# Kernel tuning notes

Hardware: AMD Instinct MI355X
Metric: run time of the kernel (lower is better)

## Reference

```python
import jax, jax.numpy as jnp
import numpy as np

ITERATION = 3
NEG = -2.0**16 + 1.0  # mask fill value from the torch code


def setup_inputs() -> dict:
    key = jax.random.key(0)
    k1, k2, k3, k4 = jax.random.split(key, 4)
    B, L, D_in, D_out, K = 1024, 512, 64, 64, 8
    low_capsule = jax.random.normal(k1, (B, L, D_in), dtype=jnp.float32)
    B_init = jax.random.normal(k2, (1, K, L), dtype=jnp.float32)
    S = jax.random.normal(k3, (D_in, D_out), dtype=jnp.float32)
    seq_len = jax.random.randint(k4, (B, 1), 1, L + 1, dtype=jnp.int32)
    return {"low_capsule": low_capsule, "B_init": B_init, "S": S, "seq_len": seq_len}


def _squash(x):
    # torch code sums squared norm over dim=1 (the capsule/max_k dim), keepdim
    sq = jnp.sum(jnp.square(x), axis=1, keepdims=True)
    scale = sq / (1.0 + sq) / jnp.sqrt(sq + 1e-9)
    return scale * x


def reference(low_capsule, B_init, S, seq_len):
    # low_capsule: [B, L, D_in], B_init: [1, K, L], S: [D_in, D_out], seq_len: [B, 1]
    Bsz, L, _ = low_capsule.shape
    K = B_init.shape[1]
    # sequence mask: [B, K, L] (seq_len tiled over K)
    mask = jnp.arange(L, dtype=seq_len.dtype)[None, None, :] < seq_len[:, :, None]
    mask = jnp.broadcast_to(mask, (Bsz, K, L))
    # bilinear projection is loop-invariant; compute once
    low_new = jnp.einsum('bld,do->blo', low_capsule, S)  # [B, L, D_out]
    B_mat = B_init
    high = None
    for _ in range(ITERATION):
        logits = jnp.where(mask, B_mat, NEG)               # [B, K, L]
        W = jax.nn.softmax(logits, axis=-1)                # masked softmax
        high = _squash(jnp.einsum('bkl,blo->bko', W, low_new))  # [B, K, D_out]
        B_delta = jnp.sum(jnp.einsum('bko,blo->bkl', high, low_new),
                          axis=0, keepdims=True)           # [1, K, L]
        B_mat = B_mat + B_delta
    return high
```

## Files before the change

### kernel.cpp

```cpp
#include <hip/hip_runtime.h>

#define NEG_FILL (-65535.0f)
#define NSLOT 32

typedef __attribute__((ext_vector_type(8))) short  short8;
typedef __attribute__((ext_vector_type(4))) float  floatx4;

__device__ inline unsigned short f2bf(float f) {
    unsigned u = __float_as_uint(f);
    u += 0x7FFFu + ((u >> 16) & 1u);
    return (unsigned short)(u >> 16);
}
__device__ inline float bf2f(unsigned short h) {
    return __uint_as_float(((unsigned)h) << 16);
}

__global__ __launch_bounds__(256) void k_init(const float* __restrict__ Binit,
                                              float* __restrict__ B0,
                                              float* __restrict__ slots) {
    int i = blockIdx.x * 256 + threadIdx.x;
    slots[i] = 0.f;
    if (i < 4096) B0[i] = Binit[i];
}

__global__ __launch_bounds__(256) void k_bred(const float* __restrict__ Bcur,
                                              float* __restrict__ Bnext,
                                              float* __restrict__ slots) {
    int i = blockIdx.x * 256 + threadIdx.x;
    float s = Bcur[i];
    #pragma unroll
    for (int j = 0; j < NSLOT; ++j) {
        s += slots[j * 4096 + i];
        slots[j * 4096 + i] = 0.f;
    }
    Bnext[i] = s;
}

__device__ __forceinline__ void softmax_to_WsT(
    const float* __restrict__ Bc, int sl, int lane, int g,
    float (*WsT)[8]) {
    #pragma unroll
    for (int kk = 0; kk < 2; ++kk) {
        const int k = g + (kk << 2);
        float v[8];
        float mx = NEG_FILL;
        #pragma unroll
        for (int j = 0; j < 8; ++j) {
            int l = lane + (j << 6);
            v[j] = (l < sl) ? Bc[(k << 9) + l] : NEG_FILL;
            mx = fmaxf(mx, v[j]);
        }
        #pragma unroll
        for (int off = 32; off; off >>= 1) mx = fmaxf(mx, __shfl_xor(mx, off));
        float s = 0.f;
        #pragma unroll
        for (int j = 0; j < 8; ++j) { v[j] = expf(v[j] - mx); s += v[j]; }
        #pragma unroll
        for (int off = 32; off; off >>= 1) s += __shfl_xor(s, off);
        const float inv = 1.0f / s;
        #pragma unroll
        for (int j = 0; j < 8; ++j) WsT[lane + (j << 6)][k] = v[j] * inv;
    }
}

__device__ __forceinline__ void delta_phase(
    const unsigned short* __restrict__ lnb, const unsigned short (*Hn)[64],
    float* __restrict__ slot, int g, int m, int q) {
    short8 afragH[2];
    #pragma unroll
    for (int oh = 0; oh < 2; ++oh) {
        short8 f = {0, 0, 0, 0, 0, 0, 0, 0};
        if (m < 8) f = *(const short8*)&Hn[m][oh * 32 + q * 8];
        afragH[oh] = f;
    }
    #pragma unroll
    for (int half = 0; half < 2; ++half) {
        short8 bf[4][2];
        #pragma unroll
        for (int t2 = 0; t2 < 4; ++t2) {
            const int lt = (g << 7) + (((half << 2) + t2) << 4);
            const unsigned short* p = &lnb[((lt + m) << 6) + q * 8];
            bf[t2][0] = *(const short8*)p;
            bf[t2][1] = *(const short8*)(p + 32);
        }
        #pragma unroll
        for (int t2 = 0; t2 < 4; ++t2) {
            const int lt = (g << 7) + (((half << 2) + t2) << 4);
            floatx4 acc = {0.f, 0.f, 0.f, 0.f};
            acc = __builtin_amdgcn_mfma_f32_16x16x32_bf16(afragH[0], bf[t2][0], acc, 0, 0, 0);
            acc = __builtin_amdgcn_mfma_f32_16x16x32_bf16(afragH[1], bf[t2][1], acc, 0, 0, 0);
            if (q < 2) {
                #pragma unroll
                for (int r = 0; r < 4; ++r)
                    atomicAdd(&slot[(q * 4 + r) * 512 + lt + m], acc[r]);
            }
        }
    }
}

__global__ __launch_bounds__(256, 4) void k_fused0(
    const float* __restrict__ low,
    const float* __restrict__ S,
    const float* __restrict__ Bc,
    float* __restrict__ slots,
    const int* __restrict__ seq_len,
    unsigned short* __restrict__ ln)
{
    __shared__ __align__(16) float WsT[512][8];
    __shared__ __align__(16) float Tpart[4][8][64];
    __shared__ __align__(16) float Tred[8][64];
    __shared__ __align__(16) unsigned short Hn[8][64];

    const int t = threadIdx.x, lane = t & 63, g = t >> 6, b = blockIdx.x;
    const int m = lane & 15, q = lane >> 4;
    const int sl = seq_len[b];
    const float* lowb = low + ((size_t)b << 15);
    unsigned short* lnb = ln + ((size_t)b << 15);

    softmax_to_WsT(Bc, sl, lane, g, WsT);
    __syncthreads();

    short8 sfrag[4][2];
    #pragma unroll
    for (int nt = 0; nt < 4; ++nt)
        #pragma unroll
        for (int dh = 0; dh < 2; ++dh) {
            short8 f;
            #pragma unroll
            for (int j = 0; j < 8; ++j) {
                int d = dh * 32 + q * 8 + j;
                f[j] = (short)f2bf(S[(d << 6) + nt * 16 + m]);
            }
            sfrag[nt][dh] = f;
        }

    float Tp[8][4];
    #pragma unroll
    for (int k = 0; k < 8; ++k)
        #pragma unroll
        for (int nt = 0; nt < 4; ++nt) Tp[k][nt] = 0.f;

    for (int tt = 0; tt < 8; ++tt) {
        const int lt = (g << 7) + (tt << 4);
        short8 afrag[2];
        #pragma unroll
        for (int dh = 0; dh < 2; ++dh) {
            const float4* p =
                (const float4*)&lowb[((lt + m) << 6) + dh * 32 + q * 8];
            float4 x0 = p[0], x1 = p[1];
            short8 f;
            f[0] = (short)f2bf(x0.x); f[1] = (short)f2bf(x0.y);
            f[2] = (short)f2bf(x0.z); f[3] = (short)f2bf(x0.w);
            f[4] = (short)f2bf(x1.x); f[5] = (short)f2bf(x1.y);
            f[6] = (short)f2bf(x1.z); f[7] = (short)f2bf(x1.w);
            afrag[dh] = f;
        }
        float lnr[4][4];
        #pragma unroll
        for (int nt = 0; nt < 4; ++nt) {
            floatx4 acc = {0.f, 0.f, 0.f, 0.f};
            acc = __builtin_amdgcn_mfma_f32_16x16x32_bf16(afrag[0], sfrag[nt][0], acc, 0, 0, 0);
            acc = __builtin_amdgcn_mfma_f32_16x16x32_bf16(afrag[1], sfrag[nt][1], acc, 0, 0, 0);
            #pragma unroll
            for (int r = 0; r < 4; ++r) {
                unsigned short hb = f2bf(acc[r]);
                lnb[((size_t)(lt + (q << 2) + r) << 6) + nt * 16 + m] = hb;
                lnr[r][nt] = bf2f(hb);
            }
        }
        if (lt < sl) {
            #pragma unroll
            for (int r = 0; r < 4; ++r) {
                const int l = lt + (q << 2) + r;
                const float4 wa = *(const float4*)&WsT[l][0];
                const float4 wb = *(const float4*)&WsT[l][4];
                #pragma unroll
                for (int nt = 0; nt < 4; ++nt) {
                    const float x = lnr[r][nt];
                    Tp[0][nt] = fmaf(wa.x, x, Tp[0][nt]);
                    Tp[1][nt] = fmaf(wa.y, x, Tp[1][nt]);
                    Tp[2][nt] = fmaf(wa.z, x, Tp[2][nt]);
                    Tp[3][nt] = fmaf(wa.w, x, Tp[3][nt]);
                    Tp[4][nt] = fmaf(wb.x, x, Tp[4][nt]);
                    Tp[5][nt] = fmaf(wb.y, x, Tp[5][nt]);
                    Tp[6][nt] = fmaf(wb.z, x, Tp[6][nt]);
                    Tp[7][nt] = fmaf(wb.w, x, Tp[7][nt]);
                }
            }
        }
    }
    #pragma unroll
    for (int k = 0; k < 8; ++k)
        #pragma unroll
        for (int nt = 0; nt < 4; ++nt) {
            float v = Tp[k][nt];
            v += __shfl_xor(v, 16);
            v += __shfl_xor(v, 32);
            Tp[k][nt] = v;
        }
    #pragma unroll
    for (int k = 0; k < 8; ++k) Tpart[g][k][lane] = Tp[k][q];
    __syncthreads();

    #pragma unroll
    for (int idx = t; idx < 512; idx += 256) {
        float s = (&Tpart[0][0][0])[idx] + (&Tpart[1][0][0])[idx]
                + (&Tpart[2][0][0])[idx] + (&Tpart[3][0][0])[idx];
        (&Tred[0][0])[idx] = s;
    }
    __syncthreads();

    float sq = 0.f;
    #pragma unroll
    for (int k = 0; k < 8; ++k) { float x = Tred[k][lane]; sq = fmaf(x, x, sq); }
    const float scale = sq / (1.0f + sq) / sqrtf(sq + 1e-9f);
    Hn[g][lane]     = f2bf(scale * Tred[g][lane]);
    Hn[g + 4][lane] = f2bf(scale * Tred[g + 4][lane]);
    __syncthreads();

    delta_phase(lnb, Hn, slots + ((size_t)(b & (NSLOT - 1)) << 12), g, m, q);
}

__global__ __launch_bounds__(256, 4) void k_route2(
    const unsigned short* __restrict__ ln,
    const float* __restrict__ Bc,
    float* __restrict__ slots,
    const int* __restrict__ seq_len,
    float* __restrict__ out,
    int last)
{
    __shared__ __align__(16) float WsT[512][8];
    __shared__ __align__(16) float Tpart[4][8][64];
    __shared__ __align__(16) float Tred[8][64];
    __shared__ __align__(16) unsigned short Hn[8][64];

    const int t = threadIdx.x, lane = t & 63, g = t >> 6, b = blockIdx.x;
    const int m = lane & 15, q = lane >> 4;
    const int sl = seq_len[b];
    const unsigned short* lnb = ln + ((size_t)b << 15);

    softmax_to_WsT(Bc, sl, lane, g, WsT);
    __syncthreads();

    floatx4 Tacc[8];
    #pragma unroll
    for (int k = 0; k < 8; ++k) Tacc[k] = (floatx4){0.f, 0.f, 0.f, 0.f};
    const int l0 = g << 7;
    const int rem = sl - l0;
    int nact = (rem <= 0) ? 0 : ((rem + 31) >> 5);
    if (nact > 4) nact = 4;

    for (int ii = 0; ii < nact; ++ii) {
        uint2 u[8];
        #pragma unroll
        for (int j = 0; j < 8; ++j) {
            const int l = l0 + (ii << 5) + (j << 2) + q;
            u[j] = *(const uint2*)&lnb[(l << 6) + (m << 2)];
        }
        #pragma unroll
        for (int j = 0; j < 8; ++j) {
            const int l = l0 + (ii << 5) + (j << 2) + q;
            const float x0 = __uint_as_float(u[j].x << 16);
            const float x1 = __uint_as_float(u[j].x & 0xFFFF0000u);
            const float x2 = __uint_as_float(u[j].y << 16);
            const float x3 = __uint_as_float(u[j].y & 0xFFFF0000u);
            const float4 wa = *(const float4*)&WsT[l][0];
            const float4 wb = *(const float4*)&WsT[l][4];
#define TROW(K, WV)                                          \
            Tacc[K][0] = fmaf(WV, x0, Tacc[K][0]);           \
            Tacc[K][1] = fmaf(WV, x1, Tacc[K][1]);           \
            Tacc[K][2] = fmaf(WV, x2, Tacc[K][2]);           \
            Tacc[K][3] = fmaf(WV, x3, Tacc[K][3]);
            TROW(0, wa.x) TROW(1, wa.y) TROW(2, wa.z) TROW(3, wa.w)
            TROW(4, wb.x) TROW(5, wb.y) TROW(6, wb.z) TROW(7, wb.w)
#undef TROW
        }
    }
    #pragma unroll
    for (int k = 0; k < 8; ++k)
        #pragma unroll
        for (int j = 0; j < 4; ++j) {
            float v = Tacc[k][j];
            v += __shfl_xor(v, 16);
            v += __shfl_xor(v, 32);
            Tacc[k][j] = v;
        }
    if (q == 0) {
        #pragma unroll
        for (int k = 0; k < 8; ++k)
            *(float4*)&Tpart[g][k][m << 2] =
                make_float4(Tacc[k][0], Tacc[k][1], Tacc[k][2], Tacc[k][3]);
    }
    __syncthreads();

    #pragma unroll
    for (int idx = t; idx < 512; idx += 256) {
        float s = (&Tpart[0][0][0])[idx] + (&Tpart[1][0][0])[idx]
                + (&Tpart[2][0][0])[idx] + (&Tpart[3][0][0])[idx];
        (&Tred[0][0])[idx] = s;
    }
    __syncthreads();

    float sq = 0.f;
    #pragma unroll
    for (int k = 0; k < 8; ++k) { float x = Tred[k][lane]; sq = fmaf(x, x, sq); }
    const float scale = sq / (1.0f + sq) / sqrtf(sq + 1e-9f);
    const float hf0 = scale * Tred[g][lane];
    const float hf1 = scale * Tred[g + 4][lane];

    if (last) {
        out[(((size_t)b * 8 + g)     << 6) + lane] = hf0;
        out[(((size_t)b * 8 + g + 4) << 6) + lane] = hf1;
        return;
    }
    Hn[g][lane]     = f2bf(hf0);
    Hn[g + 4][lane] = f2bf(hf1);
    __syncthreads();

    delta_phase(lnb, Hn, slots + ((size_t)(b & (NSLOT - 1)) << 12), g, m, q);
}

__global__ __launch_bounds__(256) void k_copy4k(const float* __restrict__ src,
                                                float* __restrict__ dst) {
    int i = blockIdx.x * 256 + threadIdx.x;
    dst[i] = src[i];
}

__global__ __launch_bounds__(256, 4) void k_route(
    const float* __restrict__ low, const float* __restrict__ S,
    const float* __restrict__ Bcur, float* __restrict__ Bnext,
    const int* __restrict__ seq_len, float* __restrict__ out, int last)
{
    __shared__ float smemA[64 * 65];
    __shared__ float Spad[64][65];
    __shared__ float GT[64][8];
    __shared__ float Tred[8][64];
    float* WsT = smemA;
    float (*Tpart)[8][64] = (float (*)[8][64])smemA;
    float (*tile)[65]     = (float (*)[65])smemA;

    const int t = threadIdx.x, o = t & 63, g = t >> 6, b = blockIdx.x;
    const int sl = seq_len[b];
    const float* lowb = low + ((size_t)b << 15);

    #pragma unroll
    for (int i = 0; i < 16; ++i) {
        int idx = t + (i << 8);
        Spad[idx >> 6][idx & 63] = S[idx];
    }
    #pragma unroll
    for (int kk = 0; kk < 2; ++kk) {
        const int k = g + (kk << 2);
        float v[8];
        float mx = NEG_FILL;
        #pragma unroll
        for (int j = 0; j < 8; ++j) {
            int l = o + (j << 6);
            v[j] = (l < sl) ? Bcur[(k << 9) + l] : NEG_FILL;
            mx = fmaxf(mx, v[j]);
        }
        #pragma unroll
        for (int off = 32; off; off >>= 1) mx = fmaxf(mx, __shfl_xor(mx, off));
        float s = 0.f;
        #pragma unroll
        for (int j = 0; j < 8; ++j) { v[j] = expf(v[j] - mx); s += v[j]; }
        #pragma unroll
        for (int off = 32; off; off >>= 1) s += __shfl_xor(s, off);
        const float inv = 1.0f / s;
        #pragma unroll
        for (int j = 0; j < 8; ++j) WsT[((o + (j << 6)) << 3) + k] = v[j] * inv;
    }
    __syncthreads();

    float Ta[8];
    #pragma unroll
    for (int k = 0; k < 8; ++k) Ta[k] = 0.f;
    {
        const int l0 = g << 7;
        #pragma unroll 4
        for (int i = 0; i < 128; ++i) {
            const int l = l0 + i;
            const float x = lowb[(l << 6) + o];
            const float4 wa = *(const float4*)&WsT[(l << 3)];
            const float4 wb = *(const float4*)&WsT[(l << 3) + 4];
            Ta[0] = fmaf(wa.x, x, Ta[0]); Ta[1] = fmaf(wa.y, x, Ta[1]);
            Ta[2] = fmaf(wa.z, x, Ta[2]); Ta[3] = fmaf(wa.w, x, Ta[3]);
            Ta[4] = fmaf(wb.x, x, Ta[4]); Ta[5] = fmaf(wb.y, x, Ta[5]);
            Ta[6] = fmaf(wb.z, x, Ta[6]); Ta[7] = fmaf(wb.w, x, Ta[7]);
        }
    }
    __syncthreads();
    #pragma unroll
    for (int k = 0; k < 8; ++k) Tpart[g][k][o] = Ta[k];
    __syncthreads();

    float h0 = 0.f, h1 = 0.f;
    #pragma unroll
    for (int gg = 0; gg < 4; ++gg) { h0 += Tpart[gg][g][o]; h1 += Tpart[gg][g + 4][o]; }
    Tred[g][o] = h0; Tred[g + 4][o] = h1;
    __syncthreads();

    float hp0 = 0.f, hp1 = 0.f;
    #pragma unroll
    for (int d = 0; d < 64; ++d) {
        const float sv = Spad[d][o];
        hp0 = fmaf(Tred[g][d], sv, hp0);
        hp1 = fmaf(Tred[g + 4][d], sv, hp1);
    }
    __syncthreads();
    Tred[g][o] = hp0; Tred[g + 4][o] = hp1;
    __syncthreads();

    float sq = 0.f;
    #pragma unroll
    for (int k = 0; k < 8; ++k) { float x = Tred[k][o]; sq = fmaf(x, x, sq); }
    const float scale = sq / (1.0f + sq) / sqrtf(sq + 1e-9f);
    const float hf0 = scale * hp0;
    const float hf1 = scale * hp1;

    if (last) {
        out[(((size_t)b * 8 + g)     << 6) + o] = hf0;
        out[(((size_t)b * 8 + g + 4) << 6) + o] = hf1;
        return;
    }
    __syncthreads();
    Tred[g][o] = hf0; Tred[g + 4][o] = hf1;
    __syncthreads();

    float g0 = 0.f, g1 = 0.f;
    #pragma unroll
    for (int oo = 0; oo < 64; ++oo) {
        const float sv = Spad[o][oo];
        g0 = fmaf(Tred[g][oo], sv, g0);
        g1 = fmaf(Tred[g + 4][oo], sv, g1);
    }
    GT[o][g] = g0; GT[o][g + 4] = g1;
    __syncthreads();

    for (int c = 0; c < 8; ++c) {
        const int lc = c << 6;
        #pragma unroll
        for (int r = 0; r < 16; ++r) {
            const int lr = (g << 4) + r;
            tile[lr][o] = lowb[((lc + lr) << 6) + o];
        }
        __syncthreads();
        float a0 = 0.f, a1 = 0.f;
        #pragma unroll
        for (int d = 0; d < 64; ++d) {
            const float x = tile[o][d];
            a0 = fmaf(GT[d][g], x, a0);
            a1 = fmaf(GT[d][g + 4], x, a1);
        }
        atomicAdd(&Bnext[(g << 9) + lc + o], a0);
        atomicAdd(&Bnext[((g + 4) << 9) + lc + o], a1);
        __syncthreads();
    }
}

extern "C" void kernel_launch(void* const* d_in, const int* in_sizes, int n_in,
                              void* d_out, int out_size, void* d_ws, size_t ws_size,
                              hipStream_t stream) {
    const float* low   = (const float*)d_in[0];
    const float* Binit = (const float*)d_in[1];
    const float* S     = (const float*)d_in[2];
    const int*   seq   = (const int*)d_in[3];
    float* outp = (float*)d_out;

    const size_t LN_BYTES   = (size_t)1024 * 512 * 64 * 2;
    const size_t SLOT_BYTES = (size_t)NSLOT * 4096 * sizeof(float);
    const size_t NEED = LN_BYTES + SLOT_BYTES + 2 * 4096 * sizeof(float);

    if (ws_size >= NEED) {
        unsigned short* lnw = (unsigned short*)d_ws;
        float* slots = (float*)((char*)d_ws + LN_BYTES);
        float* B0 = slots + (size_t)NSLOT * 4096;
        float* B1 = B0 + 4096;

        k_init<<<(NSLOT * 4096) / 256, 256, 0, stream>>>(Binit, B0, slots);

        k_fused0<<<1024, 256, 0, stream>>>(low, S, B0, slots, seq, lnw);
        k_bred<<<16, 256, 0, stream>>>(B0, B1, slots);

        k_route2<<<1024, 256, 0, stream>>>(lnw, B1, slots, seq, outp, 0);
        k_bred<<<16, 256, 0, stream>>>(B1, B0, slots);

        k_route2<<<1024, 256, 0, stream>>>(lnw, B0, nullptr, seq, outp, 1);
    } else {
        float* B0 = (float*)d_ws;
        float* B1 = B0 + 4096;
        k_copy4k<<<16, 256, 0, stream>>>(Binit, B0);
        k_copy4k<<<16, 256, 0, stream>>>(B0, B1);
        k_route<<<1024, 256, 0, stream>>>(low, S, B0, B1, seq, outp, 0);
        k_copy4k<<<16, 256, 0, stream>>>(B1, B0);
        k_route<<<1024, 256, 0, stream>>>(low, S, B1, B0, seq, outp, 0);
        k_route<<<1024, 256, 0, stream>>>(low, S, B0, nullptr, seq, outp, 1);
    }
}
```

Baseline: 295.7 us.

## Split delta phase into separate higher-occupancy kernel over half-sequence blocks

The B_delta computation moves out of the fused route kernels into a standalone k_delta kernel. It launches 2048 blocks, each covering half of a batch row's sequence, with launch bounds allowing 8 blocks per CU. The high capsules are written in fp32 to the output buffer and re-read and packed to bf16 by k_delta. The lt<sl guard in the projection kernel is also removed, so masked rows are accumulated unconditionally. This relies on softmax weights there being zero. The intent is better occupancy and parallelism for the atomic-heavy delta phase, at the cost of extra launches and an extra global round trip for the high capsules.

```diff
diff --git a/kernel.cpp b/kernel.cpp
--- a/kernel.cpp
+++ b/kernel.cpp
@@ -13,6 +13,14 @@
 }
 __device__ inline float bf2f(unsigned short h) {
     return __uint_as_float(((unsigned)h) << 16);
+}
+__device__ __forceinline__ short8 pack8(float4 a, float4 b) {
+    short8 f;
+    f[0] = (short)f2bf(a.x); f[1] = (short)f2bf(a.y);
+    f[2] = (short)f2bf(a.z); f[3] = (short)f2bf(a.w);
+    f[4] = (short)f2bf(b.x); f[5] = (short)f2bf(b.y);
+    f[6] = (short)f2bf(b.z); f[7] = (short)f2bf(b.w);
+    return f;
 }
 
 __global__ __launch_bounds__(256) void k_init(const float* __restrict__ Binit,
@@ -63,53 +71,17 @@
     }
 }
 
-__device__ __forceinline__ void delta_phase(
-    const unsigned short* __restrict__ lnb, const unsigned short (*Hn)[64],
-    float* __restrict__ slot, int g, int m, int q) {
-    short8 afragH[2];
-    #pragma unroll
-    for (int oh = 0; oh < 2; ++oh) {
-        short8 f = {0, 0, 0, 0, 0, 0, 0, 0};
-        if (m < 8) f = *(const short8*)&Hn[m][oh * 32 + q * 8];
-        afragH[oh] = f;
-    }
-    #pragma unroll
-    for (int half = 0; half < 2; ++half) {
-        short8 bf[4][2];
-        #pragma unroll
-        for (int t2 = 0; t2 < 4; ++t2) {
-            const int lt = (g << 7) + (((half << 2) + t2) << 4);
-            const unsigned short* p = &lnb[((lt + m) << 6) + q * 8];
-            bf[t2][0] = *(const short8*)p;
-            bf[t2][1] = *(const short8*)(p + 32);
-        }
-        #pragma unroll
-        for (int t2 = 0; t2 < 4; ++t2) {
-            const int lt = (g << 7) + (((half << 2) + t2) << 4);
-            floatx4 acc = {0.f, 0.f, 0.f, 0.f};
-            acc = __builtin_amdgcn_mfma_f32_16x16x32_bf16(afragH[0], bf[t2][0], acc, 0, 0, 0);
-            acc = __builtin_amdgcn_mfma_f32_16x16x32_bf16(afragH[1], bf[t2][1], acc, 0, 0, 0);
-            if (q < 2) {
-                #pragma unroll
-                for (int r = 0; r < 4; ++r)
-                    atomicAdd(&slot[(q * 4 + r) * 512 + lt + m], acc[r]);
-            }
-        }
-    }
-}
-
-__global__ __launch_bounds__(256, 4) void k_fused0(
+__global__ __launch_bounds__(256, 4) void k_lnT(
     const float* __restrict__ low,
     const float* __restrict__ S,
     const float* __restrict__ Bc,
-    float* __restrict__ slots,
     const int* __restrict__ seq_len,
-    unsigned short* __restrict__ ln)
+    unsigned short* __restrict__ ln,
+    float* __restrict__ hout)
 {
     __shared__ __align__(16) float WsT[512][8];
     __shared__ __align__(16) float Tpart[4][8][64];
     __shared__ __align__(16) float Tred[8][64];
-    __shared__ __align__(16) unsigned short Hn[8][64];
 
     const int t = threadIdx.x, lane = t & 63, g = t >> 6, b = blockIdx.x;
     const int m = lane & 15, q = lane >> 4;
@@ -168,24 +140,22 @@
                 lnr[r][nt] = bf2f(hb);
             }
         }
-        if (lt < sl) {
+        #pragma unroll
+        for (int r = 0; r < 4; ++r) {
+            const int l = lt + (q << 2) + r;
+            const float4 wa = *(const float4*)&WsT[l][0];
+            const float4 wb = *(const float4*)&WsT[l][4];
             #pragma unroll
-            for (int r = 0; r < 4; ++r) {
-                const int l = lt + (q << 2) + r;
-                const float4 wa = *(const float4*)&WsT[l][0];
-                const float4 wb = *(const float4*)&WsT[l][4];
-                #pragma unroll
-                for (int nt = 0; nt < 4; ++nt) {
-                    const float x = lnr[r][nt];
-                    Tp[0][nt] = fmaf(wa.x, x, Tp[0][nt]);
-                    Tp[1][nt] = fmaf(wa.y, x, Tp[1][nt]);
-                    Tp[2][nt] = fmaf(wa.z, x, Tp[2][nt]);
-                    Tp[3][nt] = fmaf(wa.w, x, Tp[3][nt]);
-                    Tp[4][nt] = fmaf(wb.x, x, Tp[4][nt]);
-                    Tp[5][nt] = fmaf(wb.y, x, Tp[5][nt]);
-                    Tp[6][nt] = fmaf(wb.z, x, Tp[6][nt]);
-                    Tp[7][nt] = fmaf(wb.w, x, Tp[7][nt]);
-                }
+            for (int nt = 0; nt < 4; ++nt) {
+                const float x = lnr[r][nt];
+                Tp[0][nt] = fmaf(wa.x, x, Tp[0][nt]);
+                Tp[1][nt] = fmaf(wa.y, x, Tp[1][nt]);
+                Tp[2][nt] = fmaf(wa.z, x, Tp[2][nt]);
+                Tp[3][nt] = fmaf(wa.w, x, Tp[3][nt]);
+                Tp[4][nt] = fmaf(wb.x, x, Tp[4][nt]);
+                Tp[5][nt] = fmaf(wb.y, x, Tp[5][nt]);
+                Tp[6][nt] = fmaf(wb.z, x, Tp[6][nt]);
+                Tp[7][nt] = fmaf(wb.w, x, Tp[7][nt]);
             }
         }
     }
@@ -214,25 +184,19 @@
     #pragma unroll
     for (int k = 0; k < 8; ++k) { float x = Tred[k][lane]; sq = fmaf(x, x, sq); }
     const float scale = sq / (1.0f + sq) / sqrtf(sq + 1e-9f);
-    Hn[g][lane]     = f2bf(scale * Tred[g][lane]);
-    Hn[g + 4][lane] = f2bf(scale * Tred[g + 4][lane]);
-    __syncthreads();
-
-    delta_phase(lnb, Hn, slots + ((size_t)(b & (NSLOT - 1)) << 12), g, m, q);
-}
-
-__global__ __launch_bounds__(256, 4) void k_route2(
+    hout[((size_t)b << 9) + (g << 6) + lane]       = scale * Tred[g][lane];
+    hout[((size_t)b << 9) + ((g + 4) << 6) + lane] = scale * Tred[g + 4][lane];
+}
+
+__global__ __launch_bounds__(256, 4) void k_T(
     const unsigned short* __restrict__ ln,
     const float* __restrict__ Bc,
-    float* __restrict__ slots,
     const int* __restrict__ seq_len,
-    float* __restrict__ out,
-    int last)
+    float* __restrict__ hout)
 {
     __shared__ __align__(16) float WsT[512][8];
     __shared__ __align__(16) float Tpart[4][8][64];
     __shared__ __align__(16) float Tred[8][64];
-    __shared__ __align__(16) unsigned short Hn[8][64];
 
     const int t = threadIdx.x, lane = t & 63, g = t >> 6, b = blockIdx.x;
     const int m = lane & 15, q = lane >> 4;
@@ -305,19 +269,56 @@
     #pragma unroll
     for (int k = 0; k < 8; ++k) { float x = Tred[k][lane]; sq = fmaf(x, x, sq); }
     const float scale = sq / (1.0f + sq) / sqrtf(sq + 1e-9f);
-    const float hf0 = scale * Tred[g][lane];
-    const float hf1 = scale * Tred[g + 4][lane];
-
-    if (last) {
-        out[(((size_t)b * 8 + g)     << 6) + lane] = hf0;
-        out[(((size_t)b * 8 + g + 4) << 6) + lane] = hf1;
-        return;
-    }
-    Hn[g][lane]     = f2bf(hf0);
-    Hn[g + 4][lane] = f2bf(hf1);
-    __syncthreads();
-
-    delta_phase(lnb, Hn, slots + ((size_t)(b & (NSLOT - 1)) << 12), g, m, q);
+    hout[((size_t)b << 9) + (g << 6) + lane]       = scale * Tred[g][lane];
+    hout[((size_t)b << 9) + ((g + 4) << 6) + lane] = scale * Tred[g + 4][lane];
+}
+
+__global__ __launch_bounds__(256, 8) void k_delta(
+    const unsigned short* __restrict__ ln,
+    const float* __restrict__ hout,
+    float* __restrict__ slots)
+{
+    const int t = threadIdx.x, lane = t & 63, g = t >> 6;
+    const int bb = blockIdx.x, b = bb >> 1, half = bb & 1;
+    const int m = lane & 15, q = lane >> 4;
+    const unsigned short* lnb = ln + ((size_t)b << 15);
+    const float* hb = hout + ((size_t)b << 9);
+    float* slot = slots + ((size_t)(b & (NSLOT - 1)) << 12);
+
+    short8 afragH[2];
+    #pragma unroll
+    for (int oh = 0; oh < 2; ++oh) {
+        short8 f = {0, 0, 0, 0, 0, 0, 0, 0};
+        if (m < 8) {
+            const float4* p = (const float4*)&hb[(m << 6) + oh * 32 + q * 8];
+            f = pack8(p[0], p[1]);
+        }
+        afragH[oh] = f;
+    }
+    const int lbase = (half << 8) + (g << 6);
+    #pragma unroll
+    for (int pp = 0; pp < 2; ++pp) {
+        short8 bf[2][2];
+        #pragma unroll
+        for (int u = 0; u < 2; ++u) {
+            const int lt = lbase + (((pp << 1) + u) << 4);
+            const unsigned short* p = &lnb[((lt + m) << 6) + q * 8];
+            bf[u][0] = *(const short8*)p;
+            bf[u][1] = *(const short8*)(p + 32);
+        }
+        #pragma unroll
+        for (int u = 0; u < 2; ++u) {
+            const int lt = lbase + (((pp << 1) + u) << 4);
+            floatx4 acc = {0.f, 0.f, 0.f, 0.f};
+            acc = __builtin_amdgcn_mfma_f32_16x16x32_bf16(afragH[0], bf[u][0], acc, 0, 0, 0);
+            acc = __builtin_amdgcn_mfma_f32_16x16x32_bf16(afragH[1], bf[u][1], acc, 0, 0, 0);
+            if (q < 2) {
+                #pragma unroll
+                for (int r = 0; r < 4; ++r)
+                    atomicAdd(&slot[((q << 2) + r) * 512 + lt + m], acc[r]);
+            }
+        }
+    }
 }
 
 __global__ __launch_bounds__(256) void k_copy4k(const float* __restrict__ src,
@@ -479,13 +480,15 @@
 
         k_init<<<(NSLOT * 4096) / 256, 256, 0, stream>>>(Binit, B0, slots);
 
-        k_fused0<<<1024, 256, 0, stream>>>(low, S, B0, slots, seq, lnw);
+        k_lnT<<<1024, 256, 0, stream>>>(low, S, B0, seq, lnw, outp);
+        k_delta<<<2048, 256, 0, stream>>>(lnw, outp, slots);
         k_bred<<<16, 256, 0, stream>>>(B0, B1, slots);
 
-        k_route2<<<1024, 256, 0, stream>>>(lnw, B1, slots, seq, outp, 0);
+        k_T<<<1024, 256, 0, stream>>>(lnw, B1, seq, outp);
+        k_delta<<<2048, 256, 0, stream>>>(lnw, outp, slots);
         k_bred<<<16, 256, 0, stream>>>(B1, B0, slots);
 
-        k_route2<<<1024, 256, 0, stream>>>(lnw, B0, nullptr, seq, outp, 1);
+        k_T<<<1024, 256, 0, stream>>>(lnw, B0, seq, outp);
     } else {
         float* B0 = (float*)d_ws;
         float* B1 = B0 + 4096;
```

After: 282.9 us. 4.3% less time.

## Split routing kernels per sequence half and separate delta phase into own kernel

Applied to the files above, without the earlier changes.

Each batch's routing work is split across two blocks handling halves of the sequence, with partial T sums written to a global buffer and combined later. The delta (agreement) update and final squash move into separate kernels (k_delta, k_fin), and occupancy hints rise to 6 and 8 blocks per CU. The aim is more parallelism and occupancy with less shared memory per block. The cost is extra launches, a global round trip for the partial sums, and a second read of ln in the delta kernel. k_lnT also drops the sequence-length skip on its accumulation loop, so it does some extra FMA work on masked positions.

```diff
diff --git a/kernel.cpp b/kernel.cpp
--- a/kernel.cpp
+++ b/kernel.cpp
@@ -36,8 +36,8 @@
     Bnext[i] = s;
 }
 
-__device__ __forceinline__ void softmax_to_WsT(
-    const float* __restrict__ Bc, int sl, int lane, int g,
+__device__ __forceinline__ void softmax_half(
+    const float* __restrict__ Bc, int sl, int lane, int g, int lh,
     float (*WsT)[8]) {
     #pragma unroll
     for (int kk = 0; kk < 2; ++kk) {
@@ -59,65 +59,30 @@
         for (int off = 32; off; off >>= 1) s += __shfl_xor(s, off);
         const float inv = 1.0f / s;
         #pragma unroll
-        for (int j = 0; j < 8; ++j) WsT[lane + (j << 6)][k] = v[j] * inv;
-    }
-}
-
-__device__ __forceinline__ void delta_phase(
-    const unsigned short* __restrict__ lnb, const unsigned short (*Hn)[64],
-    float* __restrict__ slot, int g, int m, int q) {
-    short8 afragH[2];
-    #pragma unroll
-    for (int oh = 0; oh < 2; ++oh) {
-        short8 f = {0, 0, 0, 0, 0, 0, 0, 0};
-        if (m < 8) f = *(const short8*)&Hn[m][oh * 32 + q * 8];
-        afragH[oh] = f;
-    }
-    #pragma unroll
-    for (int half = 0; half < 2; ++half) {
-        short8 bf[4][2];
-        #pragma unroll
-        for (int t2 = 0; t2 < 4; ++t2) {
-            const int lt = (g << 7) + (((half << 2) + t2) << 4);
-            const unsigned short* p = &lnb[((lt + m) << 6) + q * 8];
-            bf[t2][0] = *(const short8*)p;
-            bf[t2][1] = *(const short8*)(p + 32);
-        }
-        #pragma unroll
-        for (int t2 = 0; t2 < 4; ++t2) {
-            const int lt = (g << 7) + (((half << 2) + t2) << 4);
-            floatx4 acc = {0.f, 0.f, 0.f, 0.f};
-            acc = __builtin_amdgcn_mfma_f32_16x16x32_bf16(afragH[0], bf[t2][0], acc, 0, 0, 0);
-            acc = __builtin_amdgcn_mfma_f32_16x16x32_bf16(afragH[1], bf[t2][1], acc, 0, 0, 0);
-            if (q < 2) {
-                #pragma unroll
-                for (int r = 0; r < 4; ++r)
-                    atomicAdd(&slot[(q * 4 + r) * 512 + lt + m], acc[r]);
-            }
-        }
-    }
-}
-
-__global__ __launch_bounds__(256, 4) void k_fused0(
+        for (int jj = 0; jj < 4; ++jj)
+            WsT[lane + (jj << 6)][k] = v[(lh << 2) + jj] * inv;
+    }
+}
+
+__global__ __launch_bounds__(256, 6) void k_lnT(
     const float* __restrict__ low,
     const float* __restrict__ S,
     const float* __restrict__ Bc,
-    float* __restrict__ slots,
     const int* __restrict__ seq_len,
-    unsigned short* __restrict__ ln)
+    unsigned short* __restrict__ ln,
+    float* __restrict__ Tp)
 {
-    __shared__ __align__(16) float WsT[512][8];
+    __shared__ __align__(16) float WsT[256][8];
     __shared__ __align__(16) float Tpart[4][8][64];
-    __shared__ __align__(16) float Tred[8][64];
-    __shared__ __align__(16) unsigned short Hn[8][64];
-
-    const int t = threadIdx.x, lane = t & 63, g = t >> 6, b = blockIdx.x;
+
+    const int t = threadIdx.x, lane = t & 63, g = t >> 6;
+    const int bb = blockIdx.x, b = bb >> 1, lh = bb & 1;
     const int m = lane & 15, q = lane >> 4;
     const int sl = seq_len[b];
     const float* lowb = low + ((size_t)b << 15);
     unsigned short* lnb = ln + ((size_t)b << 15);
 
-    softmax_to_WsT(Bc, sl, lane, g, WsT);
+    softmax_half(Bc, sl, lane, g, lh, WsT);
     __syncthreads();
 
     short8 sfrag[4][2];
@@ -134,14 +99,14 @@
             sfrag[nt][dh] = f;
         }
 
-    float Tp[8][4];
+    float Ta[8][4];
     #pragma unroll
     for (int k = 0; k < 8; ++k)
         #pragma unroll
-        for (int nt = 0; nt < 4; ++nt) Tp[k][nt] = 0.f;
-
-    for (int tt = 0; tt < 8; ++tt) {
-        const int lt = (g << 7) + (tt << 4);
+        for (int nt = 0; nt < 4; ++nt) Ta[k][nt] = 0.f;
+
+    for (int tt = 0; tt < 4; ++tt) {
+        const int lt = (lh << 8) + (g << 6) + (tt << 4);
         short8 afrag[2];
         #pragma unroll
         for (int dh = 0; dh < 2; ++dh) {
@@ -168,24 +133,22 @@
                 lnr[r][nt] = bf2f(hb);
             }
         }
-        if (lt < sl) {
+        const int lloc = (g << 6) + (tt << 4) + (q << 2);
+        #pragma unroll
+        for (int r = 0; r < 4; ++r) {
+            const float4 wa = *(const float4*)&WsT[lloc + r][0];
+            const float4 wb = *(const float4*)&WsT[lloc + r][4];
             #pragma unroll
-            for (int r = 0; r < 4; ++r) {
-                const int l = lt + (q << 2) + r;
-                const float4 wa = *(const float4*)&WsT[l][0];
-                const float4 wb = *(const float4*)&WsT[l][4];
-                #pragma unroll
-                for (int nt = 0; nt < 4; ++nt) {
-                    const float x = lnr[r][nt];
-                    Tp[0][nt] = fmaf(wa.x, x, Tp[0][nt]);
-                    Tp[1][nt] = fmaf(wa.y, x, Tp[1][nt]);
-                    Tp[2][nt] = fmaf(wa.z, x, Tp[2][nt]);
-                    Tp[3][nt] = fmaf(wa.w, x, Tp[3][nt]);
-                    Tp[4][nt] = fmaf(wb.x, x, Tp[4][nt]);
-                    Tp[5][nt] = fmaf(wb.y, x, Tp[5][nt]);
-                    Tp[6][nt] = fmaf(wb.z, x, Tp[6][nt]);
-                    Tp[7][nt] = fmaf(wb.w, x, Tp[7][nt]);
-                }
+            for (int nt = 0; nt < 4; ++nt) {
+                const float x = lnr[r][nt];
+                Ta[0][nt] = fmaf(wa.x, x, Ta[0][nt]);
+                Ta[1][nt] = fmaf(wa.y, x, Ta[1][nt]);
+                Ta[2][nt] = fmaf(wa.z, x, Ta[2][nt]);
+                Ta[3][nt] = fmaf(wa.w, x, Ta[3][nt]);
+                Ta[4][nt] = fmaf(wb.x, x, Ta[4][nt]);
+                Ta[5][nt] = fmaf(wb.y, x, Ta[5][nt]);
+                Ta[6][nt] = fmaf(wb.z, x, Ta[6][nt]);
+                Ta[7][nt] = fmaf(wb.w, x, Ta[7][nt]);
             }
         }
     }
@@ -193,62 +156,49 @@
     for (int k = 0; k < 8; ++k)
         #pragma unroll
         for (int nt = 0; nt < 4; ++nt) {
-            float v = Tp[k][nt];
+            float v = Ta[k][nt];
             v += __shfl_xor(v, 16);
             v += __shfl_xor(v, 32);
-            Tp[k][nt] = v;
-        }
-    #pragma unroll
-    for (int k = 0; k < 8; ++k) Tpart[g][k][lane] = Tp[k][q];
+            Ta[k][nt] = v;
+        }
+    #pragma unroll
+    for (int k = 0; k < 8; ++k) Tpart[g][k][lane] = Ta[k][q];
     __syncthreads();
 
     #pragma unroll
     for (int idx = t; idx < 512; idx += 256) {
         float s = (&Tpart[0][0][0])[idx] + (&Tpart[1][0][0])[idx]
                 + (&Tpart[2][0][0])[idx] + (&Tpart[3][0][0])[idx];
-        (&Tred[0][0])[idx] = s;
-    }
-    __syncthreads();
-
-    float sq = 0.f;
-    #pragma unroll
-    for (int k = 0; k < 8; ++k) { float x = Tred[k][lane]; sq = fmaf(x, x, sq); }
-    const float scale = sq / (1.0f + sq) / sqrtf(sq + 1e-9f);
-    Hn[g][lane]     = f2bf(scale * Tred[g][lane]);
-    Hn[g + 4][lane] = f2bf(scale * Tred[g + 4][lane]);
-    __syncthreads();
-
-    delta_phase(lnb, Hn, slots + ((size_t)(b & (NSLOT - 1)) << 12), g, m, q);
-}
-
-__global__ __launch_bounds__(256, 4) void k_route2(
+        Tp[(size_t)lh * 524288 + ((size_t)b << 9) + idx] = s;
+    }
+}
+
+__global__ __launch_bounds__(256, 6) void k_T(
     const unsigned short* __restrict__ ln,
     const float* __restrict__ Bc,
-    float* __restrict__ slots,
     const int* __restrict__ seq_len,
-    float* __restrict__ out,
-    int last)
+    float* __restrict__ Tp)
 {
-    __shared__ __align__(16) float WsT[512][8];
+    __shared__ __align__(16) float WsT[256][8];
     __shared__ __align__(16) float Tpart[4][8][64];
-    __shared__ __align__(16) float Tred[8][64];
-    __shared__ __align__(16) unsigned short Hn[8][64];
-
-    const int t = threadIdx.x, lane = t & 63, g = t >> 6, b = blockIdx.x;
+
+    const int t = threadIdx.x, lane = t & 63, g = t >> 6;
+    const int bb = blockIdx.x, b = bb >> 1, lh = bb & 1;
     const int m = lane & 15, q = lane >> 4;
     const int sl = seq_len[b];
     const unsigned short* lnb = ln + ((size_t)b << 15);
 
-    softmax_to_WsT(Bc, sl, lane, g, WsT);
+    softmax_half(Bc, sl, lane, g, lh, WsT);
     __syncthreads();
 
     floatx4 Tacc[8];
     #pragma unroll
     for (int k = 0; k < 8; ++k) Tacc[k] = (floatx4){0.f, 0.f, 0.f, 0.f};
-    const int l0 = g << 7;
+    const int l0 = (lh << 8) + (g << 6);
+    const int lloc0 = g << 6;
     const int rem = sl - l0;
     int nact = (rem <= 0) ? 0 : ((rem + 31) >> 5);
-    if (nact > 4) nact = 4;
+    if (nact > 2) nact = 2;
 
     for (int ii = 0; ii < nact; ++ii) {
         uint2 u[8];
@@ -259,13 +209,13 @@
         }
         #pragma unroll
         for (int j = 0; j < 8; ++j) {
-            const int l = l0 + (ii << 5) + (j << 2) + q;
+            const int lloc = lloc0 + (ii << 5) + (j << 2) + q;
             const float x0 = __uint_as_float(u[j].x << 16);
             const float x1 = __uint_as_float(u[j].x & 0xFFFF0000u);
             const float x2 = __uint_as_float(u[j].y << 16);
             const float x3 = __uint_as_float(u[j].y & 0xFFFF0000u);
-            const float4 wa = *(const float4*)&WsT[l][0];
-            const float4 wb = *(const float4*)&WsT[l][4];
+            const float4 wa = *(const float4*)&WsT[lloc][0];
+            const float4 wb = *(const float4*)&WsT[lloc][4];
 #define TROW(K, WV)                                          \
             Tacc[K][0] = fmaf(WV, x0, Tacc[K][0]);           \
             Tacc[K][1] = fmaf(WV, x1, Tacc[K][1]);           \
@@ -297,27 +247,81 @@
     for (int idx = t; idx < 512; idx += 256) {
         float s = (&Tpart[0][0][0])[idx] + (&Tpart[1][0][0])[idx]
                 + (&Tpart[2][0][0])[idx] + (&Tpart[3][0][0])[idx];
-        (&Tred[0][0])[idx] = s;
-    }
-    __syncthreads();
-
+        Tp[(size_t)lh * 524288 + ((size_t)b << 9) + idx] = s;
+    }
+}
+
+__global__ __launch_bounds__(256, 8) void k_delta(
+    const unsigned short* __restrict__ ln,
+    const float* __restrict__ Tp,
+    float* __restrict__ slots)
+{
+    __shared__ __align__(16) float Tl[512];
+    __shared__ __align__(16) unsigned short Hn[8][64];
+
+    const int t = threadIdx.x, lane = t & 63, g = t >> 6;
+    const int bb = blockIdx.x, b = bb >> 1, half = bb & 1;
+    const int m = lane & 15, q = lane >> 4;
+    const unsigned short* lnb = ln + ((size_t)b << 15);
+    float* slot = slots + ((size_t)(b & (NSLOT - 1)) << 12);
+
+    const size_t tb = (size_t)b << 9;
+    Tl[t]       = Tp[tb + t]       + Tp[524288 + tb + t];
+    Tl[t + 256] = Tp[tb + t + 256] + Tp[524288 + tb + t + 256];
+    __syncthreads();
+    if (t < 64) {
+        float sq = 0.f;
+        #pragma unroll
+        for (int k = 0; k < 8; ++k) { float x = Tl[(k << 6) + t]; sq = fmaf(x, x, sq); }
+        const float scale = sq / (1.0f + sq) / sqrtf(sq + 1e-9f);
+        #pragma unroll
+        for (int k = 0; k < 8; ++k) Hn[k][t] = f2bf(scale * Tl[(k << 6) + t]);
+    }
+    __syncthreads();
+
+    short8 afragH[2];
+    #pragma unroll
+    for (int oh = 0; oh < 2; ++oh) {
+        short8 f = {0, 0, 0, 0, 0, 0, 0, 0};
+        if (m < 8) f = *(const short8*)&Hn[m][oh * 32 + q * 8];
+        afragH[oh] = f;
+    }
+    const int lbase = (half << 8) + (g << 6);
+    short8 bf[4][2];
+    #pragma unroll
+    for (int t2 = 0; t2 < 4; ++t2) {
+        const int lt = lbase + (t2 << 4);
+        const unsigned short* p = &lnb[((lt + m) << 6) + q * 8];
+        bf[t2][0] = *(const short8*)p;
+        bf[t2][1] = *(const short8*)(p + 32);
+    }
+    #pragma unroll
+    for (int t2 = 0; t2 < 4; ++t2) {
+        const int lt = lbase + (t2 << 4);
+        floatx4 acc = {0.f, 0.f, 0.f, 0.f};
+        acc = __builtin_amdgcn_mfma_f32_16x16x32_bf16(afragH[0], bf[t2][0], acc, 0, 0, 0);
+        acc = __builtin_amdgcn_mfma_f32_16x16x32_bf16(afragH[1], bf[t2][1], acc, 0, 0, 0);
+        if (q < 2) {
+            #pragma unroll
+            for (int r = 0; r < 4; ++r)
+                atomicAdd(&slot[((q << 2) + r) * 512 + lt + m], acc[r]);
+        }
+    }
+}
+
+__global__ __launch_bounds__(512) void k_fin(const float* __restrict__ Tp,
+                                             float* __restrict__ out) {
+    __shared__ float Tl[512];
+    const int b = blockIdx.x, t = threadIdx.x;
+    const size_t tb = (size_t)b << 9;
+    Tl[t] = Tp[tb + t] + Tp[524288 + tb + t];
+    __syncthreads();
+    const int o = t & 63;
     float sq = 0.f;
     #pragma unroll
-    for (int k = 0; k < 8; ++k) { float x = Tred[k][lane]; sq = fmaf(x, x, sq); }
+    for (int k = 0; k < 8; ++k) { float x = Tl[(k << 6) + o]; sq = fmaf(x, x, sq); }
     const float scale = sq / (1.0f + sq) / sqrtf(sq + 1e-9f);
-    const float hf0 = scale * Tred[g][lane];
-    const float hf1 = scale * Tred[g + 4][lane];
-
-    if (last) {
-        out[(((size_t)b * 8 + g)     << 6) + lane] = hf0;
-        out[(((size_t)b * 8 + g + 4) << 6) + lane] = hf1;
-        return;
-    }
-    Hn[g][lane]     = f2bf(hf0);
-    Hn[g + 4][lane] = f2bf(hf1);
-    __syncthreads();
-
-    delta_phase(lnb, Hn, slots + ((size_t)(b & (NSLOT - 1)) << 12), g, m, q);
+    out[tb + t] = scale * Tl[t];
 }
 
 __global__ __launch_bounds__(256) void k_copy4k(const float* __restrict__ src,
@@ -469,23 +473,28 @@
 
     const size_t LN_BYTES   = (size_t)1024 * 512 * 64 * 2;
     const size_t SLOT_BYTES = (size_t)NSLOT * 4096 * sizeof(float);
-    const size_t NEED = LN_BYTES + SLOT_BYTES + 2 * 4096 * sizeof(float);
+    const size_t TP_BYTES   = (size_t)2 * 1024 * 512 * sizeof(float);
+    const size_t NEED = LN_BYTES + SLOT_BYTES + 2 * 4096 * sizeof(float) + TP_BYTES;
 
     if (ws_size >= NEED) {
         unsigned short* lnw = (unsigned short*)d_ws;
         float* slots = (float*)((char*)d_ws + LN_BYTES);
         float* B0 = slots + (size_t)NSLOT * 4096;
         float* B1 = B0 + 4096;
+        float* Tp = B1 + 4096;
 
         k_init<<<(NSLOT * 4096) / 256, 256, 0, stream>>>(Binit, B0, slots);
 
-        k_fused0<<<1024, 256, 0, stream>>>(low, S, B0, slots, seq, lnw);
+        k_lnT<<<2048, 256, 0, stream>>>(low, S, B0, seq, lnw, Tp);
+        k_delta<<<2048, 256, 0, stream>>>(lnw, Tp, slots);
         k_bred<<<16, 256, 0, stream>>>(B0, B1, slots);
 
-        k_route2<<<1024, 256, 0, stream>>>(lnw, B1, slots, seq, outp, 0);
+        k_T<<<2048, 256, 0, stream>>>(lnw, B1, seq, Tp);
+        k_delta<<<2048, 256, 0, stream>>>(lnw, Tp, slots);
         k_bred<<<16, 256, 0, stream>>>(B1, B0, slots);
 
-        k_route2<<<1024, 256, 0, stream>>>(lnw, B0, nullptr, seq, outp, 1);
+        k_T<<<2048, 256, 0, stream>>>(lnw, B0, seq, Tp);
+        k_fin<<<1024, 512, 0, stream>>>(Tp, outp);
     } else {
         float* B0 = (float*)d_ws;
         float* B1 = B0 + 4096;
```

Measured after the change: 371.1 us. 1.25x slower.
